# Kernel optimization log

Hardware: AMD Instinct MI355X
Metric: run time of the kernel (lower is better)

## Reference

```python
import jax, jax.numpy as jnp
import numpy as np

EPS = 1e-6
LN_EPS = 1e-6


def _bd(x, W):
    # Block-diagonal dense: x (B, F) viewed as (B, H, D); W (H, D, D)
    B = x.shape[0]
    H, D, _ = W.shape
    return jnp.einsum('bhd,hde->bhe', x.reshape(B, H, D), W).reshape(B, H * D)


def setup_inputs() -> dict:
    key = jax.random.key(0)
    B, F, H, D, K = 4096, 1024, 4, 256, 4
    ks = jax.random.split(key, 24)
    inp = {}
    inp['inputs'] = jax.random.normal(ks[0], (B, F), jnp.float32)
    inp['c'] = jax.random.normal(ks[1], (B, F), jnp.float32)
    inp['n'] = jax.random.uniform(ks[2], (B, F), jnp.float32)  # nonzero -> general stabilizer branch
    inp['m'] = jax.random.normal(ks[3], (B, F), jnp.float32)
    inp['h'] = jax.random.normal(ks[4], (B, F), jnp.float32)
    inp['conv_state'] = jax.random.normal(ks[5], (B, K, F), jnp.float32)
    inp['conv_kernel'] = jax.random.normal(ks[6], (K, F), jnp.float32) * 0.1
    inp['conv_bias'] = jax.random.normal(ks[7], (F,), jnp.float32) * 0.1
    for idx, name in enumerate(['Wi', 'Wf', 'Wz', 'Wo', 'Ri', 'Rf', 'Rz', 'Ro']):
        inp[name] = jax.random.normal(ks[8 + idx], (H, D, D), jnp.float32) * 0.02
    for idx, name in enumerate(['bi', 'bf', 'bz', 'bo']):
        inp[name] = jax.random.normal(ks[16 + idx], (F,), jnp.float32) * 0.1
    inp['ln_scale'] = jnp.ones((H, D), jnp.float32)
    return inp


def reference(inputs, c, n, m, h, conv_state, conv_kernel, conv_bias,
              Wi, Wf, Wz, Wo, Ri, Rf, Rz, Ro, bi, bf, bz, bo, ln_scale):
    B = inputs.shape[0]
    H, D = ln_scale.shape

    # Causal depthwise conv, single step: shift state, append new input
    new_conv_state = jnp.concatenate([conv_state[:, 1:, :], inputs[:, None, :]], axis=1)  # (B,K,F)
    conv_x = jnp.einsum('bkf,kf->bf', new_conv_state, conv_kernel) + conv_bias
    conv_act = jax.nn.silu(conv_x)

    # Gate pre-activations: input (block-diag) + recurrent (block-diag) + bias
    i = _bd(conv_act, Wi) + _bd(h, Ri) + bi
    f = _bd(conv_act, Wf) + _bd(h, Rf) + bf
    z = _bd(inputs, Wz) + _bd(h, Rz) + bz
    o = _bd(inputs, Wo) + _bd(h, Ro) + bo

    o_gate = jax.nn.sigmoid(o)
    log_f = -jax.nn.softplus(-f)  # forget_activation == 'sigmoid'

    # Stabilizer
    m_new = jnp.where(jnp.all(n == 0.0), i, jnp.maximum(log_f + m, i))
    i_p = jnp.minimum(jnp.exp(i - m_new), 1.0)
    f_p = jnp.minimum(jnp.exp(log_f + m - m_new), 1.0)

    c_new = f_p * c + i_p * jnp.tanh(z)
    n_new = f_p * n + i_p
    h_new = o_gate * (c_new / jnp.maximum(n_new, EPS))

    # Multi-head LayerNorm over head_dim (scale only, no bias)
    y = h_new.reshape(B, H, D)
    mu = jnp.mean(y, axis=-1, keepdims=True)
    var = jnp.var(y, axis=-1, keepdims=True)
    out = ((y - mu) * jax.lax.rsqrt(var + LN_EPS) * ln_scale).reshape(B, H * D)

    return (out, c_new, n_new, m_new, h_new, new_conv_state)
```

## Files before the change

### kernel.cpp

```cpp
#include <hip/hip_runtime.h>

#define B_N 4096
#define F_N 1024
#define H_N 4
#define D_N 256
#define BF_ELEMS (B_N * F_N)

typedef unsigned short u16;
typedef __bf16 bf16x8 __attribute__((ext_vector_type(8)));
typedef float f32x4 __attribute__((ext_vector_type(4)));
typedef u16 u16x4 __attribute__((ext_vector_type(4)));

__device__ __forceinline__ u16 f2bf(float v) {
    union { float f; unsigned u; } x; x.f = v;
    unsigned r = x.u + 0x7fffu + ((x.u >> 16) & 1u);
    return (u16)(r >> 16);
}

__device__ __forceinline__ float bf2f(u16 v) {
    union { unsigned u; float f; } x; x.u = ((unsigned)v) << 16;
    return x.f;
}

__global__ void kzero_flag(int* flag) {
    if (threadIdx.x == 0) *flag = 0;
}

__global__ void kflag(const float* __restrict__ n, int* __restrict__ flag) {
    int idx = blockIdx.x * 256 + threadIdx.x;
    const f32x4 v = *(const f32x4*)(n + idx * 4);
    bool any = (v[0] != 0.f) || (v[1] != 0.f) || (v[2] != 0.f) || (v[3] != 0.f);
    unsigned long long msk = __ballot(any);
    if (msk && (threadIdx.x & 63) == 0) *flag = 1;
}

__global__ void kconv(const float* __restrict__ inputs, const float* __restrict__ cs,
                      const float* __restrict__ ck, const float* __restrict__ cb,
                      const float* __restrict__ h,
                      float* __restrict__ ncs_out, u16* __restrict__ convact,
                      u16* __restrict__ hbf, u16* __restrict__ inbf) {
    int idx = blockIdx.x * 256 + threadIdx.x;
    int flat = idx << 2;
    int b = flat >> 10;
    int f = flat & 1023;
    const f32x4 x  = *(const f32x4*)(inputs + flat);
    const f32x4 c1 = *(const f32x4*)(cs + b * 4096 + 1024 + f);
    const f32x4 c2 = *(const f32x4*)(cs + b * 4096 + 2048 + f);
    const f32x4 c3 = *(const f32x4*)(cs + b * 4096 + 3072 + f);
    const f32x4 k0 = *(const f32x4*)(ck + f);
    const f32x4 k1 = *(const f32x4*)(ck + 1024 + f);
    const f32x4 k2 = *(const f32x4*)(ck + 2048 + f);
    const f32x4 k3 = *(const f32x4*)(ck + 3072 + f);
    const f32x4 bias = *(const f32x4*)(cb + f);
    const f32x4 h4 = *(const f32x4*)(h + flat);

    u16x4 ca, hb, ib;
    #pragma unroll
    for (int q = 0; q < 4; ++q) {
        float v = c1[q] * k0[q] + c2[q] * k1[q] + c3[q] * k2[q] + x[q] * k3[q] + bias[q];
        float a = v / (1.f + expf(-v));
        ca[q] = f2bf(a);
        hb[q] = f2bf(h4[q]);
        ib[q] = f2bf(x[q]);
    }
    *(u16x4*)(convact + flat) = ca;
    *(u16x4*)(hbf + flat) = hb;
    *(u16x4*)(inbf + flat) = ib;

    float* ob = ncs_out + b * 4096 + f;
    *(f32x4*)(ob)        = c1;
    *(f32x4*)(ob + 1024) = c2;
    *(f32x4*)(ob + 2048) = c3;
    *(f32x4*)(ob + 3072) = x;
}

__global__ void kconvw(const float* W0, const float* W1, const float* W2, const float* W3,
                       const float* W4, const float* W5, const float* W6, const float* W7,
                       u16* __restrict__ wt) {
    const float* tab[8] = {W0, W1, W2, W3, W4, W5, W6, W7};
    int mat = blockIdx.z;
    int hd = blockIdx.y;
    const float* src = tab[mat] + hd * 65536;
    u16* dst = wt + (mat * 4 + hd) * 65536;
    __shared__ float tile[32][33];
    int tx = threadIdx.x & 31, ty = threadIdx.x >> 5;
    int bx = (blockIdx.x & 7) * 32;
    int by = (blockIdx.x >> 3) * 32;
    #pragma unroll
    for (int r = 0; r < 4; ++r)
        tile[ty + r * 8][tx] = src[(by + ty + r * 8) * 256 + bx + tx];
    __syncthreads();
    #pragma unroll
    for (int r = 0; r < 4; ++r)
        dst[(bx + ty + r * 8) * 256 + by + tx] = f2bf(tile[tx][ty + r * 8]);
}

__global__ __launch_bounds__(256) void kgemm(
    const u16* __restrict__ convact, const u16* __restrict__ inbf,
    const u16* __restrict__ hbf, const u16* __restrict__ wt,
    const float* __restrict__ bgi, const float* __restrict__ bgf,
    const float* __restrict__ bgz, const float* __restrict__ bgo,
    u16* __restrict__ gates16) {
    __shared__ u16 ldsA[128 * 32];
    __shared__ u16 ldsB[128 * 32];

    int t = threadIdx.x;
    int mtile = blockIdx.x;
    int nt = blockIdx.y;
    int z = blockIdx.z;
    int pass = z >> 2;
    int hd = z & 3;
    int gsel = pass * 2 + (nt >> 1);
    int e0 = (nt & 1) * 128;
    int row0 = mtile * 128;

    const u16* a0 = (pass ? inbf : convact) + row0 * 1024 + hd * 256;
    const u16* a1 = hbf + row0 * 1024 + hd * 256;
    const u16* b0 = wt + (gsel * 4 + hd) * 65536 + e0 * 256;
    const u16* b1 = wt + ((gsel + 4) * 4 + hd) * 65536 + e0 * 256;
    const float* btab[4] = {bgi, bgf, bgz, bgo};
    const float* bias = btab[gsel] + hd * 256 + e0;

    f32x4 acc[4][4];
    #pragma unroll
    for (int i = 0; i < 4; ++i)
        #pragma unroll
        for (int j = 0; j < 4; ++j)
            acc[i][j] = (f32x4){0.f, 0.f, 0.f, 0.f};

    int lane = t & 63;
    int lr = lane & 15, lk = lane >> 4;
    int w = t >> 6;
    int wm = w >> 1, wn = w & 1;
    int wbase = t & ~63;

    for (int ks = 0; ks < 16; ++ks) {
        int kk = ks * 32;
        const u16* ap = (kk < 256) ? (a0 + kk) : (a1 + (kk - 256));
        const u16* bp = (kk < 256) ? (b0 + kk) : (b1 + (kk - 256));
        __syncthreads();
        #pragma unroll
        for (int s = 0; s < 2; ++s) {
            int idx = t + s * 256;
            int row = idx >> 2, seg = idx & 3;
            __builtin_amdgcn_global_load_lds(
                (const __attribute__((address_space(1))) void*)(ap + row * 1024 + seg * 8),
                (__attribute__((address_space(3))) void*)(&ldsA[(wbase + s * 256) * 8]),
                16, 0, 0);
        }
        #pragma unroll
        for (int s = 0; s < 2; ++s) {
            int idx = t + s * 256;
            int row = idx >> 2, seg = idx & 3;
            __builtin_amdgcn_global_load_lds(
                (const __attribute__((address_space(1))) void*)(bp + row * 256 + seg * 8),
                (__attribute__((address_space(3))) void*)(&ldsB[(wbase + s * 256) * 8]),
                16, 0, 0);
        }
        __syncthreads();

        bf16x8 a[4], bfr[4];
        #pragma unroll
        for (int mi = 0; mi < 4; ++mi)
            a[mi] = *(const bf16x8*)&ldsA[(wm * 64 + mi * 16 + lr) * 32 + lk * 8];
        #pragma unroll
        for (int ni = 0; ni < 4; ++ni)
            bfr[ni] = *(const bf16x8*)&ldsB[(wn * 64 + ni * 16 + lr) * 32 + lk * 8];
        #pragma unroll
        for (int mi = 0; mi < 4; ++mi)
            #pragma unroll
            for (int ni = 0; ni < 4; ++ni)
                acc[mi][ni] = __builtin_amdgcn_mfma_f32_16x16x32_bf16(a[mi], bfr[ni], acc[mi][ni], 0, 0, 0);
    }

    float bv[4];
    #pragma unroll
    for (int ni = 0; ni < 4; ++ni)
        bv[ni] = bias[wn * 64 + ni * 16 + lr];

    u16* gout = gates16 + (size_t)gsel * BF_ELEMS;
    #pragma unroll
    for (int mi = 0; mi < 4; ++mi)
        #pragma unroll
        for (int ni = 0; ni < 4; ++ni)
            #pragma unroll
            for (int r = 0; r < 4; ++r) {
                int row = row0 + wm * 64 + mi * 16 + lk * 4 + r;
                int col = hd * 256 + e0 + wn * 64 + ni * 16 + lr;
                gout[row * 1024 + col] = f2bf(acc[mi][ni][r] + bv[ni]);
            }
}

__global__ __launch_bounds__(256) void kpoint(
    const u16* __restrict__ gates16,
    const float* __restrict__ c, const float* __restrict__ n, const float* __restrict__ m,
    const float* __restrict__ ln_scale, const int* __restrict__ flagp,
    float* __restrict__ out) {
    int b = blockIdx.x;
    int t = threadIdx.x;
    int l = t & 63;
    int j = (t >> 6) * 256 + l * 4;
    int idx = b * 1024 + j;
    int flag = *flagp;

    u16x4 iv = *(const u16x4*)(gates16 + idx);
    u16x4 fv = *(const u16x4*)(gates16 + (size_t)BF_ELEMS + idx);
    u16x4 zv = *(const u16x4*)(gates16 + 2 * (size_t)BF_ELEMS + idx);
    u16x4 ov = *(const u16x4*)(gates16 + 3 * (size_t)BF_ELEMS + idx);
    f32x4 cv = *(const f32x4*)(c + idx);
    f32x4 nv = *(const f32x4*)(n + idx);
    f32x4 mv = *(const f32x4*)(m + idx);
    f32x4 sc = *(const f32x4*)(ln_scale + j);

    f32x4 cn, nn, mn, hn;
    float s = 0.f, ss = 0.f;
    #pragma unroll
    for (int q = 0; q < 4; ++q) {
        float I = bf2f(iv[q]);
        float Fg = bf2f(fv[q]);
        float Z = bf2f(zv[q]);
        float O = bf2f(ov[q]);
        float og = 1.f / (1.f + expf(-O));
        float lf = (Fg >= 0.f) ? -log1pf(expf(-Fg)) : (Fg - log1pf(expf(Fg)));
        float mnew = flag ? fmaxf(lf + mv[q], I) : I;
        float ip = fminf(expf(I - mnew), 1.f);
        float fp = fminf(expf(lf + mv[q] - mnew), 1.f);
        float cnew = fp * cv[q] + ip * tanhf(Z);
        float nnew = fp * nv[q] + ip;
        float hnew = og * (cnew / fmaxf(nnew, 1e-6f));
        cn[q] = cnew; nn[q] = nnew; mn[q] = mnew; hn[q] = hnew;
        s += hnew; ss += hnew * hnew;
    }
    #pragma unroll
    for (int off = 32; off >= 1; off >>= 1) {
        s  += __shfl_xor(s, off);
        ss += __shfl_xor(ss, off);
    }
    float mu = s * (1.f / 256.f);
    float var = ss * (1.f / 256.f) - mu * mu;
    float rs = rsqrtf(var + 1e-6f);

    f32x4 o4;
    #pragma unroll
    for (int q = 0; q < 4; ++q)
        o4[q] = (hn[q] - mu) * rs * sc[q];

    *(f32x4*)(out + idx) = o4;
    *(f32x4*)(out + (size_t)BF_ELEMS + idx) = cn;
    *(f32x4*)(out + 2 * (size_t)BF_ELEMS + idx) = nn;
    *(f32x4*)(out + 3 * (size_t)BF_ELEMS + idx) = mn;
    *(f32x4*)(out + 4 * (size_t)BF_ELEMS + idx) = hn;
}

extern "C" void kernel_launch(void* const* d_in, const int* in_sizes, int n_in,
                              void* d_out, int out_size, void* d_ws, size_t ws_size,
                              hipStream_t stream) {
    const float* inputs = (const float*)d_in[0];
    const float* c = (const float*)d_in[1];
    const float* n = (const float*)d_in[2];
    const float* m = (const float*)d_in[3];
    const float* h = (const float*)d_in[4];
    const float* conv_state = (const float*)d_in[5];
    const float* conv_kernel = (const float*)d_in[6];
    const float* conv_bias = (const float*)d_in[7];
    const float* W[8];
    for (int i = 0; i < 8; ++i) W[i] = (const float*)d_in[8 + i];
    const float* bgi = (const float*)d_in[16];
    const float* bgf = (const float*)d_in[17];
    const float* bgz = (const float*)d_in[18];
    const float* bgo = (const float*)d_in[19];
    const float* ln_scale = (const float*)d_in[20];
    float* out = (float*)d_out;

    char* ws = (char*)d_ws;
    int* flag = (int*)ws;
    u16* convact = (u16*)(ws + 256);
    u16* hbf = convact + BF_ELEMS;
    u16* inbf = hbf + BF_ELEMS;
    u16* wt = inbf + BF_ELEMS;
    u16* gates16 = wt + (size_t)8 * 4 * 65536;

    kzero_flag<<<1, 64, 0, stream>>>(flag);
    kflag<<<4096, 256, 0, stream>>>(n, flag);
    kconv<<<4096, 256, 0, stream>>>(inputs, conv_state, conv_kernel, conv_bias, h,
                                    out + 5 * (size_t)BF_ELEMS, convact, hbf, inbf);
    kconvw<<<dim3(64, 4, 8), 256, 0, stream>>>(W[0], W[1], W[2], W[3], W[4], W[5], W[6], W[7], wt);
    kgemm<<<dim3(32, 4, 8), 256, 0, stream>>>(convact, inbf, hbf, wt,
                                              bgi, bgf, bgz, bgo, gates16);
    kpoint<<<4096, 256, 0, stream>>>(gates16, c, n, m, ln_scale, flag, out);
}
```

Before: 127.0 us.

## Fuse prep kernels and enlarge GEMM tile to 128x256 with K=64 steps

Merges the flag check, conv/cast, and weight transpose-cast kernels into one launch, and replaces the zero-flag kernel with a memset. The flag pass no longer needs its own kernel, so n is read alongside the other inputs. The GEMM now uses 512-thread blocks with a 128x256 output tile and a 64-wide K step, so each A tile is reused across the full head width and there are fewer barriers per output. The cost is more LDS per block and fewer blocks in the grid, which may lower occupancy.

```diff
diff --git a/kernel.cpp b/kernel.cpp
--- a/kernel.cpp
+++ b/kernel.cpp
@@ -22,104 +22,99 @@
     return x.f;
 }
 
-__global__ void kzero_flag(int* flag) {
-    if (threadIdx.x == 0) *flag = 0;
-}
-
-__global__ void kflag(const float* __restrict__ n, int* __restrict__ flag) {
-    int idx = blockIdx.x * 256 + threadIdx.x;
-    const f32x4 v = *(const f32x4*)(n + idx * 4);
-    bool any = (v[0] != 0.f) || (v[1] != 0.f) || (v[2] != 0.f) || (v[3] != 0.f);
-    unsigned long long msk = __ballot(any);
-    if (msk && (threadIdx.x & 63) == 0) *flag = 1;
-}
-
-__global__ void kconv(const float* __restrict__ inputs, const float* __restrict__ cs,
-                      const float* __restrict__ ck, const float* __restrict__ cb,
-                      const float* __restrict__ h,
-                      float* __restrict__ ncs_out, u16* __restrict__ convact,
-                      u16* __restrict__ hbf, u16* __restrict__ inbf) {
-    int idx = blockIdx.x * 256 + threadIdx.x;
-    int flat = idx << 2;
-    int b = flat >> 10;
-    int f = flat & 1023;
-    const f32x4 x  = *(const f32x4*)(inputs + flat);
-    const f32x4 c1 = *(const f32x4*)(cs + b * 4096 + 1024 + f);
-    const f32x4 c2 = *(const f32x4*)(cs + b * 4096 + 2048 + f);
-    const f32x4 c3 = *(const f32x4*)(cs + b * 4096 + 3072 + f);
-    const f32x4 k0 = *(const f32x4*)(ck + f);
-    const f32x4 k1 = *(const f32x4*)(ck + 1024 + f);
-    const f32x4 k2 = *(const f32x4*)(ck + 2048 + f);
-    const f32x4 k3 = *(const f32x4*)(ck + 3072 + f);
-    const f32x4 bias = *(const f32x4*)(cb + f);
-    const f32x4 h4 = *(const f32x4*)(h + flat);
-
-    u16x4 ca, hb, ib;
-    #pragma unroll
-    for (int q = 0; q < 4; ++q) {
-        float v = c1[q] * k0[q] + c2[q] * k1[q] + c3[q] * k2[q] + x[q] * k3[q] + bias[q];
-        float a = v / (1.f + expf(-v));
-        ca[q] = f2bf(a);
-        hb[q] = f2bf(h4[q]);
-        ib[q] = f2bf(x[q]);
-    }
-    *(u16x4*)(convact + flat) = ca;
-    *(u16x4*)(hbf + flat) = hb;
-    *(u16x4*)(inbf + flat) = ib;
-
-    float* ob = ncs_out + b * 4096 + f;
-    *(f32x4*)(ob)        = c1;
-    *(f32x4*)(ob + 1024) = c2;
-    *(f32x4*)(ob + 2048) = c3;
-    *(f32x4*)(ob + 3072) = x;
-}
-
-__global__ void kconvw(const float* W0, const float* W1, const float* W2, const float* W3,
-                       const float* W4, const float* W5, const float* W6, const float* W7,
-                       u16* __restrict__ wt) {
-    const float* tab[8] = {W0, W1, W2, W3, W4, W5, W6, W7};
-    int mat = blockIdx.z;
-    int hd = blockIdx.y;
-    const float* src = tab[mat] + hd * 65536;
-    u16* dst = wt + (mat * 4 + hd) * 65536;
+__global__ __launch_bounds__(256) void kprep(
+    const float* __restrict__ inputs, const float* __restrict__ cs,
+    const float* __restrict__ ck, const float* __restrict__ cb,
+    const float* __restrict__ h, const float* __restrict__ n,
+    const float* W0, const float* W1, const float* W2, const float* W3,
+    const float* W4, const float* W5, const float* W6, const float* W7,
+    float* __restrict__ ncs_out, u16* __restrict__ convact,
+    u16* __restrict__ hbf, u16* __restrict__ inbf,
+    u16* __restrict__ wt, int* __restrict__ flag) {
     __shared__ float tile[32][33];
-    int tx = threadIdx.x & 31, ty = threadIdx.x >> 5;
-    int bx = (blockIdx.x & 7) * 32;
-    int by = (blockIdx.x >> 3) * 32;
-    #pragma unroll
-    for (int r = 0; r < 4; ++r)
-        tile[ty + r * 8][tx] = src[(by + ty + r * 8) * 256 + bx + tx];
-    __syncthreads();
-    #pragma unroll
-    for (int r = 0; r < 4; ++r)
-        dst[(bx + ty + r * 8) * 256 + by + tx] = f2bf(tile[tx][ty + r * 8]);
-}
-
-__global__ __launch_bounds__(256) void kgemm(
+    int bid = blockIdx.x;
+    int t = threadIdx.x;
+    if (bid < 4096) {
+        int idx = bid * 256 + t;
+        int flat = idx << 2;
+        int b = flat >> 10;
+        int f = flat & 1023;
+        const f32x4 x  = *(const f32x4*)(inputs + flat);
+        const f32x4 c1 = *(const f32x4*)(cs + b * 4096 + 1024 + f);
+        const f32x4 c2 = *(const f32x4*)(cs + b * 4096 + 2048 + f);
+        const f32x4 c3 = *(const f32x4*)(cs + b * 4096 + 3072 + f);
+        const f32x4 k0 = *(const f32x4*)(ck + f);
+        const f32x4 k1 = *(const f32x4*)(ck + 1024 + f);
+        const f32x4 k2 = *(const f32x4*)(ck + 2048 + f);
+        const f32x4 k3 = *(const f32x4*)(ck + 3072 + f);
+        const f32x4 bias = *(const f32x4*)(cb + f);
+        const f32x4 h4 = *(const f32x4*)(h + flat);
+        const f32x4 nv = *(const f32x4*)(n + flat);
+
+        bool any = (nv[0] != 0.f) || (nv[1] != 0.f) || (nv[2] != 0.f) || (nv[3] != 0.f);
+        unsigned long long msk = __ballot(any);
+        if (msk && (t & 63) == 0) *flag = 1;
+
+        u16x4 ca, hb, ib;
+        #pragma unroll
+        for (int q = 0; q < 4; ++q) {
+            float v = c1[q] * k0[q] + c2[q] * k1[q] + c3[q] * k2[q] + x[q] * k3[q] + bias[q];
+            float a = v / (1.f + expf(-v));
+            ca[q] = f2bf(a);
+            hb[q] = f2bf(h4[q]);
+            ib[q] = f2bf(x[q]);
+        }
+        *(u16x4*)(convact + flat) = ca;
+        *(u16x4*)(hbf + flat) = hb;
+        *(u16x4*)(inbf + flat) = ib;
+
+        float* ob = ncs_out + b * 4096 + f;
+        *(f32x4*)(ob)        = c1;
+        *(f32x4*)(ob + 1024) = c2;
+        *(f32x4*)(ob + 2048) = c3;
+        *(f32x4*)(ob + 3072) = x;
+    } else {
+        int wb = bid - 4096;
+        int gx = wb & 63;
+        int hd = (wb >> 6) & 3;
+        int mat = wb >> 8;
+        const float* tab[8] = {W0, W1, W2, W3, W4, W5, W6, W7};
+        const float* src = tab[mat] + hd * 65536;
+        u16* dst = wt + (mat * 4 + hd) * 65536;
+        int tx = t & 31, ty = t >> 5;
+        int bx = (gx & 7) * 32;
+        int by = (gx >> 3) * 32;
+        #pragma unroll
+        for (int r = 0; r < 4; ++r)
+            tile[ty + r * 8][tx] = src[(by + ty + r * 8) * 256 + bx + tx];
+        __syncthreads();
+        #pragma unroll
+        for (int r = 0; r < 4; ++r)
+            dst[(bx + ty + r * 8) * 256 + by + tx] = f2bf(tile[tx][ty + r * 8]);
+    }
+}
+
+__global__ __launch_bounds__(512, 4) void kgemm(
     const u16* __restrict__ convact, const u16* __restrict__ inbf,
     const u16* __restrict__ hbf, const u16* __restrict__ wt,
     const float* __restrict__ bgi, const float* __restrict__ bgf,
     const float* __restrict__ bgz, const float* __restrict__ bgo,
     u16* __restrict__ gates16) {
-    __shared__ u16 ldsA[128 * 32];
-    __shared__ u16 ldsB[128 * 32];
+    __shared__ u16 ldsA[128 * 64];
+    __shared__ u16 ldsB[256 * 64];
 
     int t = threadIdx.x;
     int mtile = blockIdx.x;
-    int nt = blockIdx.y;
-    int z = blockIdx.z;
-    int pass = z >> 2;
-    int hd = z & 3;
-    int gsel = pass * 2 + (nt >> 1);
-    int e0 = (nt & 1) * 128;
+    int pairidx = blockIdx.y;
+    int gsel = pairidx >> 2;
+    int hd = pairidx & 3;
     int row0 = mtile * 128;
 
-    const u16* a0 = (pass ? inbf : convact) + row0 * 1024 + hd * 256;
+    const u16* a0 = (gsel >= 2 ? inbf : convact) + row0 * 1024 + hd * 256;
     const u16* a1 = hbf + row0 * 1024 + hd * 256;
-    const u16* b0 = wt + (gsel * 4 + hd) * 65536 + e0 * 256;
-    const u16* b1 = wt + ((gsel + 4) * 4 + hd) * 65536 + e0 * 256;
-    const float* btab[4] = {bgi, bgf, bgz, bgo};
-    const float* bias = btab[gsel] + hd * 256 + e0;
+    const u16* b0 = wt + (gsel * 4 + hd) * 65536;
+    const u16* b1 = wt + ((gsel + 4) * 4 + hd) * 65536;
+    const float* bias = (gsel == 0 ? bgi : gsel == 1 ? bgf : gsel == 2 ? bgz : bgo) + hd * 256;
 
     f32x4 acc[4][4];
     #pragma unroll
@@ -131,46 +126,49 @@
     int lane = t & 63;
     int lr = lane & 15, lk = lane >> 4;
     int w = t >> 6;
-    int wm = w >> 1, wn = w & 1;
+    int wm = w >> 2, wn = w & 3;
     int wbase = t & ~63;
 
-    for (int ks = 0; ks < 16; ++ks) {
-        int kk = ks * 32;
-        const u16* ap = (kk < 256) ? (a0 + kk) : (a1 + (kk - 256));
-        const u16* bp = (kk < 256) ? (b0 + kk) : (b1 + (kk - 256));
+    int arow = t >> 3, aseg = t & 7;
+
+    for (int ks = 0; ks < 8; ++ks) {
+        int kb = ks * 64;
+        const u16* ap = (kb < 256) ? (a0 + kb) : (a1 + (kb - 256));
+        const u16* bp = (kb < 256) ? (b0 + kb) : (b1 + (kb - 256));
         __syncthreads();
         #pragma unroll
         for (int s = 0; s < 2; ++s) {
-            int idx = t + s * 256;
-            int row = idx >> 2, seg = idx & 3;
+            int row = arow + s * 64;
             __builtin_amdgcn_global_load_lds(
-                (const __attribute__((address_space(1))) void*)(ap + row * 1024 + seg * 8),
-                (__attribute__((address_space(3))) void*)(&ldsA[(wbase + s * 256) * 8]),
+                (const __attribute__((address_space(1))) void*)(ap + row * 1024 + aseg * 8),
+                (__attribute__((address_space(3))) void*)(&ldsA[(wbase + s * 512) * 8]),
                 16, 0, 0);
         }
         #pragma unroll
-        for (int s = 0; s < 2; ++s) {
-            int idx = t + s * 256;
-            int row = idx >> 2, seg = idx & 3;
+        for (int s = 0; s < 4; ++s) {
+            int row = arow + s * 64;
             __builtin_amdgcn_global_load_lds(
-                (const __attribute__((address_space(1))) void*)(bp + row * 256 + seg * 8),
-                (__attribute__((address_space(3))) void*)(&ldsB[(wbase + s * 256) * 8]),
+                (const __attribute__((address_space(1))) void*)(bp + row * 256 + aseg * 8),
+                (__attribute__((address_space(3))) void*)(&ldsB[(wbase + s * 512) * 8]),
                 16, 0, 0);
         }
         __syncthreads();
 
-        bf16x8 a[4], bfr[4];
-        #pragma unroll
-        for (int mi = 0; mi < 4; ++mi)
-            a[mi] = *(const bf16x8*)&ldsA[(wm * 64 + mi * 16 + lr) * 32 + lk * 8];
-        #pragma unroll
-        for (int ni = 0; ni < 4; ++ni)
-            bfr[ni] = *(const bf16x8*)&ldsB[(wn * 64 + ni * 16 + lr) * 32 + lk * 8];
-        #pragma unroll
-        for (int mi = 0; mi < 4; ++mi)
+        #pragma unroll
+        for (int kk = 0; kk < 2; ++kk) {
+            bf16x8 a[4], bfr[4];
+            #pragma unroll
+            for (int mi = 0; mi < 4; ++mi)
+                a[mi] = *(const bf16x8*)&ldsA[(wm * 64 + mi * 16 + lr) * 64 + kk * 32 + lk * 8];
             #pragma unroll
             for (int ni = 0; ni < 4; ++ni)
-                acc[mi][ni] = __builtin_amdgcn_mfma_f32_16x16x32_bf16(a[mi], bfr[ni], acc[mi][ni], 0, 0, 0);
+                bfr[ni] = *(const bf16x8*)&ldsB[(wn * 64 + ni * 16 + lr) * 64 + kk * 32 + lk * 8];
+            #pragma unroll
+            for (int mi = 0; mi < 4; ++mi)
+                #pragma unroll
+                for (int ni = 0; ni < 4; ++ni)
+                    acc[mi][ni] = __builtin_amdgcn_mfma_f32_16x16x32_bf16(a[mi], bfr[ni], acc[mi][ni], 0, 0, 0);
+        }
     }
 
     float bv[4];
@@ -186,7 +184,7 @@
             #pragma unroll
             for (int r = 0; r < 4; ++r) {
                 int row = row0 + wm * 64 + mi * 16 + lk * 4 + r;
-                int col = hd * 256 + e0 + wn * 64 + ni * 16 + lr;
+                int col = hd * 256 + wn * 64 + ni * 16 + lr;
                 gout[row * 1024 + col] = f2bf(acc[mi][ni][r] + bv[ni]);
             }
 }
@@ -280,12 +278,11 @@
     u16* wt = inbf + BF_ELEMS;
     u16* gates16 = wt + (size_t)8 * 4 * 65536;
 
-    kzero_flag<<<1, 64, 0, stream>>>(flag);
-    kflag<<<4096, 256, 0, stream>>>(n, flag);
-    kconv<<<4096, 256, 0, stream>>>(inputs, conv_state, conv_kernel, conv_bias, h,
-                                    out + 5 * (size_t)BF_ELEMS, convact, hbf, inbf);
-    kconvw<<<dim3(64, 4, 8), 256, 0, stream>>>(W[0], W[1], W[2], W[3], W[4], W[5], W[6], W[7], wt);
-    kgemm<<<dim3(32, 4, 8), 256, 0, stream>>>(convact, inbf, hbf, wt,
-                                              bgi, bgf, bgz, bgo, gates16);
+    hipMemsetAsync(flag, 0, 4, stream);
+    kprep<<<6144, 256, 0, stream>>>(inputs, conv_state, conv_kernel, conv_bias, h, n,
+                                    W[0], W[1], W[2], W[3], W[4], W[5], W[6], W[7],
+                                    out + 5 * (size_t)BF_ELEMS, convact, hbf, inbf, wt, flag);
+    kgemm<<<dim3(32, 16), 512, 0, stream>>>(convact, inbf, hbf, wt,
+                                            bgi, bgf, bgz, bgo, gates16);
     kpoint<<<4096, 256, 0, stream>>>(gates16, c, n, m, ln_scale, flag, out);
 }
```

After: 114.4 us. -10.0%, faster.
